# Optimization experiments

Measured on AMD Instinct MI355X. Metric: run time of the kernel, lower is better.

The kernel has to match this reference:

```python
import jax, jax.numpy as jnp
import numpy as np

N_HEADS = 16

def _rotate_half(t):
    # t: [B, H, T, hs]; split last dim in half, return cat(-x2, x1)
    hs = t.shape[-1]
    x1, x2 = t[..., : hs // 2], t[..., hs // 2 :]
    return jnp.concatenate((-x2, x1), axis=-1)

def _rope_pos(T, hs, dtype):
    inv_freq = 1.0 / (10000.0 ** (jnp.arange(0, hs, 2, dtype=jnp.float32) / hs))
    freqs = jnp.arange(T, dtype=jnp.float32)[:, None] * inv_freq[None, :]  # [T, hs/2]
    pos = jnp.concatenate((freqs, freqs), axis=-1)  # [T, hs]
    return pos

def setup_inputs() -> dict:
    key = jax.random.key(0)
    ks = jax.random.split(key, 5)
    d = 2048
    x = jax.random.normal(ks[0], (2, 2048, d), dtype=jnp.float32)
    W_attn = jax.random.normal(ks[1], (d, 3 * d), dtype=jnp.float32) * (1.0 / np.sqrt(d))
    b_attn = jax.random.normal(ks[2], (3 * d,), dtype=jnp.float32) * 0.02
    W_proj = jax.random.normal(ks[3], (d, d), dtype=jnp.float32) * (1.0 / np.sqrt(d))
    b_proj = jax.random.normal(ks[4], (d,), dtype=jnp.float32) * 0.02
    return {"x": x, "W_attn": W_attn, "b_attn": b_attn, "W_proj": W_proj, "b_proj": b_proj}

def reference(x, W_attn, b_attn, W_proj, b_proj):
    B, T, C = x.shape
    nh = N_HEADS
    hs = C // nh
    qkv = x @ W_attn + b_attn  # [B, T, 3C]
    q, k, v = jnp.split(qkv, 3, axis=-1)
    # [B, T, C] -> [B, nh, T, hs]
    def to_heads(t):
        return t.reshape(B, T, nh, hs).transpose(0, 2, 1, 3)
    q, k, v = to_heads(q), to_heads(k), to_heads(v)
    # RoPE
    pos = _rope_pos(T, hs, x.dtype)  # [T, hs]
    cos, sin = jnp.cos(pos).astype(x.dtype), jnp.sin(pos).astype(x.dtype)
    q = q * cos + _rotate_half(q) * sin
    k = k * cos + _rotate_half(k) * sin
    # causal SDPA
    scale = 1.0 / np.sqrt(hs)
    scores = jnp.einsum('bhqd,bhkd->bhqk', q, k) * scale  # [B, nh, T, T]
    causal = jnp.tril(jnp.ones((T, T), dtype=bool))
    scores = jnp.where(causal, scores, jnp.finfo(scores.dtype).min)
    att = jax.nn.softmax(scores, axis=-1)
    out = jnp.einsum('bhqk,bhkd->bhqd', att, v)  # [B, nh, T, hs]
    y = out.transpose(0, 2, 1, 3).reshape(B, T, C)
    return y @ W_proj + b_proj
```

## Files before the change

kernel.cpp:

```cpp
#include <hip/hip_runtime.h>
#include <stdint.h>

typedef unsigned short u16;
typedef __attribute__((ext_vector_type(8))) short short8;
typedef __attribute__((ext_vector_type(4))) float f32x4;
typedef __attribute__((ext_vector_type(4))) unsigned short u16x4;

#define DEV __device__ __forceinline__

DEV u16 f2bf(float f) {
  union { float f; unsigned u; } v; v.f = f;
  unsigned r = v.u + 0x7fffu + ((v.u >> 16) & 1u);
  return (u16)(r >> 16);
}
DEV float bf2f(u16 b) {
  union { unsigned u; float f; } v; v.u = ((unsigned)b) << 16;
  return v.f;
}
DEV void gload_lds16(const void* g, void* l) {
  __builtin_amdgcn_global_load_lds((const __attribute__((address_space(1))) void*)g,
                                   (__attribute__((address_space(3))) void*)l,
                                   16, 0, 0);
}
DEV void block_barrier() {
  asm volatile("" ::: "memory");
  __builtin_amdgcn_s_barrier();
  asm volatile("" ::: "memory");
}

__global__ void k_prep(const float* __restrict__ x, u16* __restrict__ xb,
                       const float* __restrict__ Wa, u16* __restrict__ wqkvT,
                       const float* __restrict__ Wp, u16* __restrict__ wprojT,
                       float* __restrict__ ct, float* __restrict__ st) {
  __shared__ float tile[32][33];
  const int bid = blockIdx.x, tid = threadIdx.x;
  if (bid < 8192) {
    int i = bid * 256 + tid;
    const f32x4 v = *(const f32x4*)(x + (size_t)i * 4);
    u16x4 o;
    o[0] = f2bf(v[0]); o[1] = f2bf(v[1]); o[2] = f2bf(v[2]); o[3] = f2bf(v[3]);
    *(u16x4*)(xb + (size_t)i * 4) = o;
  } else if (bid < 8192 + 12288 + 4096) {
    const bool wa = bid < 8192 + 12288;
    const int b2 = wa ? bid - 8192 : bid - 8192 - 12288;
    const int gw = wa ? 192 : 64;
    const float* in = wa ? Wa : Wp;
    u16* out = wa ? wqkvT : wprojT;
    const int C = wa ? 6144 : 2048;
    const int c0 = (b2 % gw) * 32, r0 = (b2 / gw) * 32;
    const int tx = tid & 31, ty = tid >> 5;
#pragma unroll
    for (int j = 0; j < 32; j += 8)
      tile[ty + j][tx] = in[(size_t)(r0 + ty + j) * C + (c0 + tx)];
    __syncthreads();
#pragma unroll
    for (int j = 0; j < 32; j += 8)
      out[(size_t)(c0 + ty + j) * 2048 + (r0 + tx)] = f2bf(tile[tx][ty + j]);
  } else {
    int id = (bid - 24576) * 256 + tid;
    int t = id >> 6, dd = id & 63;
    float inv = exp2f((float)dd * -0.20762050593045077f);
    float s, c;
    sincosf((float)t * inv, &s, &c);
    ct[id] = c; st[id] = s;
  }
}

__global__ __launch_bounds__(512, 2) void k_gemmqkv(const u16* __restrict__ A,
                                                    const u16* __restrict__ Bt,
                                                    const float* __restrict__ bias,
                                                    u16* __restrict__ qh,
                                                    u16* __restrict__ kh,
                                                    u16* __restrict__ vt,
                                                    const float* __restrict__ rtab) {
  const int Kld = 2048, nt = 32;
  __shared__ __align__(16) short smem[4][256 * 64];
  const int tid = threadIdx.x;
  const int wid = tid >> 6, lane = tid & 63;
  const int gx = gridDim.x;
  const int nwg = gx * gridDim.y;
  const int orig = blockIdx.y * gx + blockIdx.x;
  const int lg = (orig & 7) * (nwg >> 3) + (orig >> 3);
  const int bm = (lg % gx) * 256, bn = (lg / gx) * 256;
  const int wr = wid >> 2, wc = wid & 3;
  const int r = lane & 15, kq = lane >> 4, r7 = lane & 7;

  int aoff[4], boff[4], lbase[4];
#pragma unroll
  for (int j = 0; j < 4; ++j) {
    int c = j * 512 + wid * 64 + lane;
    int row = c >> 3, ch = c & 7;
    aoff[j] = (bm + row) * Kld + (ch ^ (row & 7)) * 8;
    boff[j] = (bn + row) * Kld + (ch ^ (row & 7)) * 8;
    lbase[j] = (j * 512 + wid * 64) * 16;
  }

#define STG_A(k0, buf, j) gload_lds16(A + aoff[j] + (k0), (char*)&smem[(buf)][0] + lbase[j])
#define STG_B(k0, buf, j) gload_lds16(Bt + boff[j] + (k0), (char*)&smem[2 + (buf)][0] + lbase[j])
#define RD_A(AF, MH, KK)                                                        \
  _Pragma("unroll")                                                             \
  for (int m2 = 0; m2 < 4; ++m2)                                                \
    AF[m2] = *(const short8*)&As[(wr * 128 + (MH) * 64 + m2 * 16 + r) * 64      \
                                 + (((KK) * 4 + kq) ^ r7) * 8];
#define RD_B(KK)                                                                \
  _Pragma("unroll")                                                             \
  for (int nf = 0; nf < 4; ++nf)                                                \
    bfr[KK][nf] = *(const short8*)&Bs[(wc * 64 + nf * 16 + r) * 64              \
                                      + (((KK) * 4 + kq) ^ r7) * 8];
#define PH_MFMA(AF, MH, KK)                                                     \
  __builtin_amdgcn_s_setprio(1);                                                \
  _Pragma("unroll")                                                             \
  for (int m2 = 0; m2 < 4; ++m2)                                                \
    _Pragma("unroll")                                                           \
    for (int nf = 0; nf < 4; ++nf)                                              \
      acc[(MH) * 4 + m2][nf] = __builtin_amdgcn_mfma_f32_16x16x32_bf16(         \
          AF[m2], bfr[KK][nf], acc[(MH) * 4 + m2][nf], 0, 0, 0);                \
  __builtin_amdgcn_s_setprio(0);

  f32x4 acc[8][4];
  const f32x4 zero = {0.f, 0.f, 0.f, 0.f};
#pragma unroll
  for (int i = 0; i < 8; ++i)
#pragma unroll
    for (int j = 0; j < 4; ++j) acc[i][j] = zero;

#pragma unroll
  for (int j = 0; j < 4; ++j) STG_A(0, 0, j);
#pragma unroll
  for (int j = 0; j < 4; ++j) STG_B(0, 0, j);
#pragma unroll
  for (int j = 0; j < 4; ++j) STG_B(64, 1, j);
  asm volatile("s_waitcnt vmcnt(4)" ::: "memory");
  block_barrier();

#pragma unroll 1
  for (int t = 0; t < nt; ++t) {
    const int cur = t & 1, nxt = cur ^ 1;
    const short* As = &smem[cur][0];
    const short* Bs = &smem[2 + cur][0];
    const int kA = (t + 1) * 64, kB = (t + 2) * 64;
    const bool sA = (t + 1 < nt), sB = (t + 2 < nt);
    short8 bfr[2][4];
    short8 af[4];

    RD_B(0)
    RD_A(af, 0, 0)
    if (sA) { STG_A(kA, nxt, 0); STG_A(kA, nxt, 1); }
    block_barrier();
    PH_MFMA(af, 0, 0)
    block_barrier();

    RD_B(1)
    RD_A(af, 0, 1)
    if (sA) { STG_A(kA, nxt, 2); STG_A(kA, nxt, 3); }
    block_barrier();
    PH_MFMA(af, 0, 1)
    block_barrier();

    RD_A(af, 1, 0)
    if (sB) { STG_B(kB, cur, 0); STG_B(kB, cur, 1); }
    block_barrier();
    PH_MFMA(af, 1, 0)
    block_barrier();

    RD_A(af, 1, 1)
    if (sB) { STG_B(kB, cur, 2); STG_B(kB, cur, 3); }
    block_barrier();
    PH_MFMA(af, 1, 1)
    if (t + 1 < nt) {
      if (sB) asm volatile("s_waitcnt vmcnt(4)" ::: "memory");
      else    asm volatile("s_waitcnt vmcnt(0)" ::: "memory");
    }
    block_barrier();
  }
#undef STG_A
#undef STG_B
#undef RD_A
#undef RD_B
#undef PH_MFMA

  const int by = lg / gx;
  const int part = by >> 3;
  const int b_ = bm >> 11;
  const int tb = bm & 2047;
  const int hbase = (bn & 2047) >> 7;
  u16* ob = (u16*)&smem[0][0];

#pragma unroll
  for (int nf = 0; nf < 4; ++nf) {
    int nl = wc * 64 + nf * 16 + r;
    float bv = bias[bn + nl];
#pragma unroll
    for (int mf = 0; mf < 8; ++mf) {
      int mlb = wr * 128 + mf * 16 + kq * 4;
#pragma unroll
      for (int i = 0; i < 4; ++i) {
        int ml = mlb + i;
        int cl = (part == 2)
          ? (nl ^ (((ml >> 2) & 3) << 4) ^ (((ml >> 4) & 7) << 1))
          : (nl ^ (((ml >> 2) & 3) << 4));
        ob[ml * 256 + cl] = f2bf(acc[mf][nf][i] + bv);
      }
    }
  }
  block_barrier();

  if (part == 2) {
#pragma unroll 1
    for (int iter = 0; iter < 32; ++iter) {
      int dl = iter * 8 + wid;
      int hh = hbase + (dl >> 7), d = dl & 127;
      int tl4 = lane * 4;
      int cl = dl ^ ((lane & 3) << 4) ^ (((lane >> 2) & 7) << 1);
      u16x4 o;
#pragma unroll
      for (int j = 0; j < 4; ++j) o[j] = ob[(tl4 + j) * 256 + cl];
      *(u16x4*)(vt + ((size_t)(b_ * 16 + hh) * 128 + d) * 2048 + tb + tl4) = o;
    }
  } else {
    u16* dst = part ? kh : qh;
    const float qscale = part ? 1.0f : 0.12751744766834352f;
    const int nl2 = lane * 4;
    const int hh = hbase + (nl2 >> 7);
    const int d0 = nl2 & 127;
    const int hi = (nl2 >> 6) & 1;
    const int dd4 = nl2 & 63;
    const float* ct = rtab;
    const float* st = rtab + 131072;
#pragma unroll 2
    for (int iter = 0; iter < 32; ++iter) {
      int tl = iter * 8 + wid;
      int tg = tb + tl;
      f32x4 c4 = *(const f32x4*)(ct + tg * 64 + dd4);
      f32x4 s4 = *(const f32x4*)(st + tg * 64 + dd4);
      int xr = ((tl >> 2) & 3) << 4;
      int base = tl * 256 + (nl2 ^ xr);
      int pbase = tl * 256 + ((nl2 ^ 64) ^ xr);
      u16x4 o;
#pragma unroll
      for (int j = 0; j < 4; ++j) {
        float vo = bf2f(ob[base + j]);
        float vp = bf2f(ob[pbase + j]);
        float vr = hi ? (vo * c4[j] + vp * s4[j]) : (vo * c4[j] - vp * s4[j]);
        o[j] = f2bf(vr * qscale);
      }
      *(u16x4*)(dst + ((size_t)(b_ * 16 + hh) * 2048 + tg) * 128 + d0) = o;
    }
  }
}

template <bool OUT_BF16, bool SPLITK>
__global__ __launch_bounds__(512, 2) void k_gemm3(const u16* __restrict__ A,
                                                  const u16* __restrict__ Bt,
                                                  const float* __restrict__ bias,
                                                  void* __restrict__ Cv,
                                                  int M, int N, int Kld, int nkt) {
  __shared__ __align__(16) short lA[2][256 * 64];
  __shared__ __align__(16) short lB[2][256 * 64];
  const int tid = threadIdx.x;
  const int wid = tid >> 6, lane = tid & 63;
  const int gx = gridDim.x;
  const int nwg = gx * gridDim.y;
  const int orig = blockIdx.y * gx + blockIdx.x;
  const int lg = (orig & 7) * (nwg >> 3) + (orig >> 3);
  const int bm = (lg % gx) * 256, bn = (lg / gx) * 256;
  const int wr = wid >> 2, wc = wid & 3;
  const int r = lane & 15, kq = lane >> 4, r7 = lane & 7;
  const int kz = SPLITK ? blockIdx.z * (nkt << 6) : 0;

  int aoff[4], boff[4], lbase[4];
#pragma unroll
  for (int j = 0; j < 4; ++j) {
    int c = j * 512 + wid * 64 + lane;
    int row = c >> 3, ch = c & 7;
    aoff[j] = (bm + row) * Kld + kz + (ch ^ (row & 7)) * 8;
    boff[j] = (bn + row) * Kld + kz + (ch ^ (row & 7)) * 8;
    lbase[j] = (j * 512 + wid * 64) * 16;
  }

#define STG_A(k0, buf, j) gload_lds16(A + aoff[j] + (k0), (char*)&lA[(buf)][0] + lbase[j])
#define STG_B(k0, buf, j) gload_lds16(Bt + boff[j] + (k0), (char*)&lB[(buf)][0] + lbase[j])
#define RD_A(AF, MH, KK)                                                        \
  _Pragma("unroll")                                                             \
  for (int m2 = 0; m2 < 4; ++m2)                                                \
    AF[m2] = *(const short8*)&As[(wr * 128 + (MH) * 64 + m2 * 16 + r) * 64      \
                                 + (((KK) * 4 + kq) ^ r7) * 8];
#define RD_B(KK)                                                                \
  _Pragma("unroll")                                                             \
  for (int nf = 0; nf < 4; ++nf)                                                \
    bfr[KK][nf] = *(const short8*)&Bs[(wc * 64 + nf * 16 + r) * 64              \
                                      + (((KK) * 4 + kq) ^ r7) * 8];
#define PH_MFMA(AF, MH, KK)                                                     \
  __builtin_amdgcn_s_setprio(1);                                                \
  _Pragma("unroll")                                                             \
  for (int m2 = 0; m2 < 4; ++m2)                                                \
    _Pragma("unroll")                                                           \
    for (int nf = 0; nf < 4; ++nf)                                              \
      acc[(MH) * 4 + m2][nf] = __builtin_amdgcn_mfma_f32_16x16x32_bf16(         \
          AF[m2], bfr[KK][nf], acc[(MH) * 4 + m2][nf], 0, 0, 0);                \
  __builtin_amdgcn_s_setprio(0);

  f32x4 acc[8][4];
  const f32x4 zero = {0.f, 0.f, 0.f, 0.f};
#pragma unroll
  for (int i = 0; i < 8; ++i)
#pragma unroll
    for (int j = 0; j < 4; ++j) acc[i][j] = zero;

  const int nt = nkt;

#pragma unroll
  for (int j = 0; j < 4; ++j) STG_A(0, 0, j);
#pragma unroll
  for (int j = 0; j < 4; ++j) STG_B(0, 0, j);
  if (nt > 1) {
#pragma unroll
    for (int j = 0; j < 4; ++j) STG_B(64, 1, j);
    asm volatile("s_waitcnt vmcnt(4)" ::: "memory");
  } else {
    asm volatile("s_waitcnt vmcnt(0)" ::: "memory");
  }
  block_barrier();

#pragma unroll 1
  for (int t = 0; t < nt; ++t) {
    const int cur = t & 1, nxt = cur ^ 1;
    const short* As = &lA[cur][0];
    const short* Bs = &lB[cur][0];
    const int kA = (t + 1) * 64, kB = (t + 2) * 64;
    const bool sA = (t + 1 < nt), sB = (t + 2 < nt);
    short8 bfr[2][4];
    short8 af[4];

    RD_B(0)
    RD_A(af, 0, 0)
    if (sA) { STG_A(kA, nxt, 0); STG_A(kA, nxt, 1); }
    block_barrier();
    PH_MFMA(af, 0, 0)
    block_barrier();

    RD_B(1)
    RD_A(af, 0, 1)
    if (sA) { STG_A(kA, nxt, 2); STG_A(kA, nxt, 3); }
    block_barrier();
    PH_MFMA(af, 0, 1)
    block_barrier();

    RD_A(af, 1, 0)
    if (sB) { STG_B(kB, cur, 0); STG_B(kB, cur, 1); }
    block_barrier();
    PH_MFMA(af, 1, 0)
    block_barrier();

    RD_A(af, 1, 1)
    if (sB) { STG_B(kB, cur, 2); STG_B(kB, cur, 3); }
    block_barrier();
    PH_MFMA(af, 1, 1)
    if (t + 1 < nt) {
      if (sB) asm volatile("s_waitcnt vmcnt(4)" ::: "memory");
      else    asm volatile("s_waitcnt vmcnt(0)" ::: "memory");
    }
    block_barrier();
  }
#undef STG_A
#undef STG_B
#undef RD_A
#undef RD_B
#undef PH_MFMA

#pragma unroll
  for (int mf = 0; mf < 8; ++mf)
#pragma unroll
    for (int nf = 0; nf < 4; ++nf) {
      int n = bn + wc * 64 + nf * 16 + r;
      float bv = SPLITK ? 0.f : bias[n];
#pragma unroll
      for (int i = 0; i < 4; ++i) {
        int m = bm + wr * 128 + mf * 16 + kq * 4 + i;
        float val = acc[mf][nf][i] + bv;
        if (SPLITK)
          ((float*)Cv)[(size_t)blockIdx.z * M * N + (size_t)m * N + n] = val;
        else if (OUT_BF16)
          ((u16*)Cv)[(size_t)m * N + n] = f2bf(val);
        else
          ((float*)Cv)[(size_t)m * N + n] = val;
      }
    }
}

__global__ void k_fadd(const float* __restrict__ p, const float* __restrict__ bias,
                       float* __restrict__ y, int n4) {
  const int half4 = 2097152;
  for (int i = blockIdx.x * blockDim.x + threadIdx.x; i < n4; i += gridDim.x * blockDim.x) {
    f32x4 a = *(const f32x4*)(p + (size_t)i * 4);
    f32x4 b = *(const f32x4*)(p + (size_t)(i + half4) * 4);
    f32x4 bv = *(const f32x4*)(bias + ((i & 511) << 2));
    f32x4 o = a + b + bv;
    *(f32x4*)(y + (size_t)i * 4) = o;
  }
}

__global__ __launch_bounds__(256) void k_attn(const u16* __restrict__ qh,
                                              const u16* __restrict__ kh,
                                              const u16* __restrict__ vt,
                                              u16* __restrict__ out) {
  __shared__ __align__(16) short lK[2][64 * 128];
  __shared__ __align__(16) short lV[2][128 * 64];
  __shared__ __align__(16) short lP[128 * 64];
  const int tid = threadIdx.x, wid = tid >> 6, lane = tid & 63;
  const int id = blockIdx.x;
  const int jr = id & 15;
  const int J = (id < 256) ? jr : 15 - jr;
  const int h = (id >> 4) & 15, b = id >> 8;
  const int q0 = J * 128;
  const int nkt = 2 * J + 2;
  const size_t bh = (size_t)b * 16 + h;
  const u16* qb = qh + bh * 2048 * 128;
  const u16* kb = kh + bh * 2048 * 128;
  const u16* vb = vt + bh * 128 * 2048;
  const int r = lane & 15, kq = lane >> 4;
  const int r7 = r & 7;
  const int wrow = wid * 32;

  int koff[4], voff[4];
#pragma unroll
  for (int i = 0; i < 4; ++i) {
    int ci = (wid * 4 + i) * 64 + lane;
    int krow = ci >> 4, kch = ci & 15;
    koff[i] = krow * 128 + ((kch ^ (krow & 7)) * 8);
    int vrow = ci >> 3, vch = ci & 7;
    voff[i] = vrow * 2048 + ((vch ^ (vrow & 7)) * 8);
  }

  short8 qa[2][4];
#pragma unroll
  for (int mf = 0; mf < 2; ++mf)
#pragma unroll
    for (int kk = 0; kk < 4; ++kk)
      qa[mf][kk] = *(const short8*)(qb + (size_t)(q0 + wrow + mf * 16 + r) * 128 + kk * 32 + kq * 8);

  f32x4 O[2][8];
  const f32x4 zero = {0.f, 0.f, 0.f, 0.f};
#pragma unroll
  for (int mf = 0; mf < 2; ++mf)
#pragma unroll
    for (int nf = 0; nf < 8; ++nf) O[mf][nf] = zero;
  float lp[2] = {0.f, 0.f};

#pragma unroll
  for (int i = 0; i < 4; ++i) {
    gload_lds16(kb + koff[i], (char*)&lK[0][0] + (wid * 4 + i) * 1024);
    gload_lds16(vb + voff[i], (char*)&lV[0][0] + (wid * 4 + i) * 1024);
  }

#pragma unroll 1
  for (int kt = 0; kt < nkt; ++kt) {
    const int cur = kt & 1;
    if (kt + 1 < nkt) {
      const size_t kbase = (size_t)(kt + 1) * 8192, vbase = (size_t)(kt + 1) * 64;
#pragma unroll
      for (int i = 0; i < 4; ++i) {
        gload_lds16(kb + kbase + koff[i], (char*)&lK[cur ^ 1][0] + (wid * 4 + i) * 1024);
        gload_lds16(vb + vbase + voff[i], (char*)&lV[cur ^ 1][0] + (wid * 4 + i) * 1024);
      }
      asm volatile("s_waitcnt vmcnt(8)" ::: "memory");
    } else {
      asm volatile("s_waitcnt vmcnt(0)" ::: "memory");
    }
    block_barrier();

    f32x4 S[2][4];
#pragma unroll
    for (int mf = 0; mf < 2; ++mf)
#pragma unroll
      for (int nf = 0; nf < 4; ++nf) S[mf][nf] = zero;
#pragma unroll
    for (int kk = 0; kk < 4; ++kk) {
      short8 kf[4];
#pragma unroll
      for (int nf = 0; nf < 4; ++nf)
        kf[nf] = *(const short8*)&lK[cur][(nf * 16 + r) * 128 + ((kk * 4 + kq) ^ r7) * 8];
      __builtin_amdgcn_s_setprio(1);
#pragma unroll
      for (int mf = 0; mf < 2; ++mf)
#pragma unroll
        for (int nf = 0; nf < 4; ++nf)
          S[mf][nf] = __builtin_amdgcn_mfma_f32_16x16x32_bf16(kf[nf], qa[mf][kk], S[mf][nf], 0, 0, 0);
      __builtin_amdgcn_s_setprio(0);
    }

    const bool diag = (kt >= nkt - 2);
#pragma unroll
    for (int mf = 0; mf < 2; ++mf) {
      const int rl = wrow + mf * 16 + r;
#pragma unroll
      for (int nf = 0; nf < 4; ++nf) {
        float pv4[4];
#pragma unroll
        for (int i = 0; i < 4; ++i) {
          float pv = exp2f(S[mf][nf][i]);
          if (diag) {
            int kg = kt * 64 + nf * 16 + kq * 4 + i;
            int qg = q0 + wrow + mf * 16 + r;
            pv = (kg > qg) ? 0.f : pv;
          }
          lp[mf] += pv;
          pv4[i] = pv;
        }
        unsigned d0, d1;
        asm("v_cvt_pk_bf16_f32 %0, %1, %2" : "=v"(d0) : "v"(pv4[0]), "v"(pv4[1]));
        asm("v_cvt_pk_bf16_f32 %0, %1, %2" : "=v"(d1) : "v"(pv4[2]), "v"(pv4[3]));
        int g = (nf * 4 + kq) ^ (r7 << 1);
        *(uint2*)((char*)lP + rl * 128 + g * 8) = make_uint2(d0, d1);
      }
    }

#pragma unroll
    for (int kk = 0; kk < 2; ++kk) {
      short8 pa[2];
#pragma unroll
      for (int mf = 0; mf < 2; ++mf) {
        int rl = wrow + mf * 16 + r;
        int g = (kk * 8 + kq * 2) ^ (r7 << 1);
        pa[mf] = *(const short8*)((const char*)lP + rl * 128 + g * 8);
      }
#pragma unroll
      for (int nf = 0; nf < 8; ++nf) {
        short8 vf = *(const short8*)&lV[cur][(nf * 16 + r) * 64 + ((kk * 4 + kq) ^ r7) * 8];
        __builtin_amdgcn_s_setprio(1);
#pragma unroll
        for (int mf = 0; mf < 2; ++mf)
          O[mf][nf] = __builtin_amdgcn_mfma_f32_16x16x32_bf16(pa[mf], vf, O[mf][nf], 0, 0, 0);
        __builtin_amdgcn_s_setprio(0);
      }
    }
    asm volatile("s_waitcnt lgkmcnt(0)" ::: "memory");
    block_barrier();
  }

#pragma unroll
  for (int mf = 0; mf < 2; ++mf) {
    float v = lp[mf];
    v += __shfl_xor(v, 16);
    v += __shfl_xor(v, 32);
    lp[mf] = v;
  }
#pragma unroll
  for (int mf = 0; mf < 2; ++mf) {
    float inv[4];
#pragma unroll
    for (int i = 0; i < 4; ++i)
      inv[i] = 1.f / __shfl(lp[mf], kq * 4 + i, 16);
#pragma unroll
    for (int nf = 0; nf < 8; ++nf)
#pragma unroll
      for (int i = 0; i < 4; ++i) {
        int qg = q0 + wrow + mf * 16 + kq * 4 + i;
        out[(size_t)(b * 2048 + qg) * 2048 + h * 128 + nf * 16 + r] = f2bf(O[mf][nf][i] * inv[i]);
      }
  }
}

extern "C" void kernel_launch(void* const* d_in, const int* in_sizes, int n_in,
                              void* d_out, int out_size, void* d_ws, size_t ws_size,
                              hipStream_t stream) {
  const float* x      = (const float*)d_in[0];
  const float* W_attn = (const float*)d_in[1];
  const float* b_attn = (const float*)d_in[2];
  const float* W_proj = (const float*)d_in[3];
  const float* b_proj = (const float*)d_in[4];
  float* y = (float*)d_out;

  u16* xb     = (u16*)d_ws;
  u16* wqkvT  = xb     + (size_t)4096 * 2048;
  u16* wprojT = wqkvT  + (size_t)6144 * 2048;
  u16* qkv    = wprojT + (size_t)2048 * 2048;
  u16* qh     = qkv    + (size_t)4096 * 6144;
  u16* kh     = qh     + (size_t)4096 * 2048;
  u16* vt     = kh     + (size_t)4096 * 2048;
  u16* attout = vt     + (size_t)4096 * 2048;
  if (ws_size < (size_t)83886080 * 2) return;

  float* rtab  = (float*)qkv;
  float* pproj = (float*)qkv;

  k_prep<<<25088, 256, 0, stream>>>(x, xb, W_attn, wqkvT, W_proj, wprojT, rtab, rtab + 131072);
  k_gemmqkv<<<dim3(16, 24), 512, 0, stream>>>(xb, wqkvT, b_attn, qh, kh, vt, rtab);
  k_attn<<<512, 256, 0, stream>>>(qh, kh, vt, attout);
  k_gemm3<false, true><<<dim3(16, 8, 2), 512, 0, stream>>>(attout, wprojT, b_proj, pproj, 4096, 2048, 2048, 16);
  k_fadd<<<2048, 256, 0, stream>>>(pproj, b_proj, y, 2097152);
}
```

Measured before the change: 300.6 us.

## Replace split-K projection GEMM plus reduction with 256x128-tile direct-output kernel

The output projection used to run as a split-K GEMM with 256x256 tiles that wrote two fp32 partial buffers, followed by a separate kernel that summed them and added the bias. It is now a single GEMM over the full K with 256x128 tiles on a 16x16 grid, adding the bias and writing y directly. This removes the partial-sum round trip through memory and one kernel launch. In exchange each tile reuses less data per load and runs a longer K loop.

Result: faster. 291.5 us (-3.0%).

```diff
diff --git a/kernel.cpp b/kernel.cpp
--- a/kernel.cpp
+++ b/kernel.cpp
@@ -249,41 +249,43 @@
   }
 }
 
-template <bool OUT_BF16, bool SPLITK>
-__global__ __launch_bounds__(512, 2) void k_gemm3(const u16* __restrict__ A,
-                                                  const u16* __restrict__ Bt,
-                                                  const float* __restrict__ bias,
-                                                  void* __restrict__ Cv,
-                                                  int M, int N, int Kld, int nkt) {
+__global__ __launch_bounds__(512, 2) void k_proj(const u16* __restrict__ A,
+                                                 const u16* __restrict__ Bt,
+                                                 const float* __restrict__ bias,
+                                                 float* __restrict__ y) {
+  const int Kld = 2048, nt = 32;
   __shared__ __align__(16) short lA[2][256 * 64];
-  __shared__ __align__(16) short lB[2][256 * 64];
+  __shared__ __align__(16) short lB[2][128 * 64];
   const int tid = threadIdx.x;
   const int wid = tid >> 6, lane = tid & 63;
-  const int gx = gridDim.x;
-  const int nwg = gx * gridDim.y;
-  const int orig = blockIdx.y * gx + blockIdx.x;
-  const int lg = (orig & 7) * (nwg >> 3) + (orig >> 3);
-  const int bm = (lg % gx) * 256, bn = (lg / gx) * 256;
-  const int wr = wid >> 2, wc = wid & 3;
+  const int orig = blockIdx.y * 16 + blockIdx.x;
+  const int lg = (orig & 7) * 32 + (orig >> 3);
+  const int bm = (lg & 15) * 256, bn = (lg >> 4) * 128;
+  const int wr = wid >> 1, wc = wid & 1;
   const int r = lane & 15, kq = lane >> 4, r7 = lane & 7;
-  const int kz = SPLITK ? blockIdx.z * (nkt << 6) : 0;
-
-  int aoff[4], boff[4], lbase[4];
+
+  int aoff[4], boff[2], albase[4], blbase[2];
 #pragma unroll
   for (int j = 0; j < 4; ++j) {
     int c = j * 512 + wid * 64 + lane;
     int row = c >> 3, ch = c & 7;
-    aoff[j] = (bm + row) * Kld + kz + (ch ^ (row & 7)) * 8;
-    boff[j] = (bn + row) * Kld + kz + (ch ^ (row & 7)) * 8;
-    lbase[j] = (j * 512 + wid * 64) * 16;
-  }
-
-#define STG_A(k0, buf, j) gload_lds16(A + aoff[j] + (k0), (char*)&lA[(buf)][0] + lbase[j])
-#define STG_B(k0, buf, j) gload_lds16(Bt + boff[j] + (k0), (char*)&lB[(buf)][0] + lbase[j])
+    aoff[j] = (bm + row) * Kld + (ch ^ (row & 7)) * 8;
+    albase[j] = (j * 512 + wid * 64) * 16;
+  }
+#pragma unroll
+  for (int j = 0; j < 2; ++j) {
+    int c = j * 512 + wid * 64 + lane;
+    int row = c >> 3, ch = c & 7;
+    boff[j] = (bn + row) * Kld + (ch ^ (row & 7)) * 8;
+    blbase[j] = (j * 512 + wid * 64) * 16;
+  }
+
+#define STG_A(k0, buf, j) gload_lds16(A + aoff[j] + (k0), (char*)&lA[(buf)][0] + albase[j])
+#define STG_B(k0, buf, j) gload_lds16(Bt + boff[j] + (k0), (char*)&lB[(buf)][0] + blbase[j])
 #define RD_A(AF, MH, KK)                                                        \
   _Pragma("unroll")                                                             \
-  for (int m2 = 0; m2 < 4; ++m2)                                                \
-    AF[m2] = *(const short8*)&As[(wr * 128 + (MH) * 64 + m2 * 16 + r) * 64      \
+  for (int m2 = 0; m2 < 2; ++m2)                                                \
+    AF[m2] = *(const short8*)&As[(wr * 64 + (MH) * 32 + m2 * 16 + r) * 64       \
                                  + (((KK) * 4 + kq) ^ r7) * 8];
 #define RD_B(KK)                                                                \
   _Pragma("unroll")                                                             \
@@ -293,33 +295,27 @@
 #define PH_MFMA(AF, MH, KK)                                                     \
   __builtin_amdgcn_s_setprio(1);                                                \
   _Pragma("unroll")                                                             \
-  for (int m2 = 0; m2 < 4; ++m2)                                                \
+  for (int m2 = 0; m2 < 2; ++m2)                                                \
     _Pragma("unroll")                                                           \
     for (int nf = 0; nf < 4; ++nf)                                              \
-      acc[(MH) * 4 + m2][nf] = __builtin_amdgcn_mfma_f32_16x16x32_bf16(         \
-          AF[m2], bfr[KK][nf], acc[(MH) * 4 + m2][nf], 0, 0, 0);                \
+      acc[(MH) * 2 + m2][nf] = __builtin_amdgcn_mfma_f32_16x16x32_bf16(         \
+          AF[m2], bfr[KK][nf], acc[(MH) * 2 + m2][nf], 0, 0, 0);                \
   __builtin_amdgcn_s_setprio(0);
 
-  f32x4 acc[8][4];
+  f32x4 acc[4][4];
   const f32x4 zero = {0.f, 0.f, 0.f, 0.f};
 #pragma unroll
-  for (int i = 0; i < 8; ++i)
+  for (int i = 0; i < 4; ++i)
 #pragma unroll
     for (int j = 0; j < 4; ++j) acc[i][j] = zero;
 
-  const int nt = nkt;
-
 #pragma unroll
   for (int j = 0; j < 4; ++j) STG_A(0, 0, j);
 #pragma unroll
-  for (int j = 0; j < 4; ++j) STG_B(0, 0, j);
-  if (nt > 1) {
-#pragma unroll
-    for (int j = 0; j < 4; ++j) STG_B(64, 1, j);
-    asm volatile("s_waitcnt vmcnt(4)" ::: "memory");
-  } else {
-    asm volatile("s_waitcnt vmcnt(0)" ::: "memory");
-  }
+  for (int j = 0; j < 2; ++j) STG_B(0, 0, j);
+#pragma unroll
+  for (int j = 0; j < 2; ++j) STG_B(64, 1, j);
+  asm volatile("s_waitcnt vmcnt(2)" ::: "memory");
   block_barrier();
 
 #pragma unroll 1
@@ -330,7 +326,7 @@
     const int kA = (t + 1) * 64, kB = (t + 2) * 64;
     const bool sA = (t + 1 < nt), sB = (t + 2 < nt);
     short8 bfr[2][4];
-    short8 af[4];
+    short8 af[2];
 
     RD_B(0)
     RD_A(af, 0, 0)
@@ -347,17 +343,17 @@
     block_barrier();
 
     RD_A(af, 1, 0)
-    if (sB) { STG_B(kB, cur, 0); STG_B(kB, cur, 1); }
+    if (sB) STG_B(kB, cur, 0);
     block_barrier();
     PH_MFMA(af, 1, 0)
     block_barrier();
 
     RD_A(af, 1, 1)
-    if (sB) { STG_B(kB, cur, 2); STG_B(kB, cur, 3); }
+    if (sB) STG_B(kB, cur, 1);
     block_barrier();
     PH_MFMA(af, 1, 1)
     if (t + 1 < nt) {
-      if (sB) asm volatile("s_waitcnt vmcnt(4)" ::: "memory");
+      if (sB) asm volatile("s_waitcnt vmcnt(2)" ::: "memory");
       else    asm volatile("s_waitcnt vmcnt(0)" ::: "memory");
     }
     block_barrier();
@@ -369,35 +365,17 @@
 #undef PH_MFMA
 
 #pragma unroll
-  for (int mf = 0; mf < 8; ++mf)
+  for (int mf = 0; mf < 4; ++mf)
 #pragma unroll
     for (int nf = 0; nf < 4; ++nf) {
       int n = bn + wc * 64 + nf * 16 + r;
-      float bv = SPLITK ? 0.f : bias[n];
+      float bv = bias[n];
 #pragma unroll
       for (int i = 0; i < 4; ++i) {
-        int m = bm + wr * 128 + mf * 16 + kq * 4 + i;
-        float val = acc[mf][nf][i] + bv;
-        if (SPLITK)
-          ((float*)Cv)[(size_t)blockIdx.z * M * N + (size_t)m * N + n] = val;
-        else if (OUT_BF16)
-          ((u16*)Cv)[(size_t)m * N + n] = f2bf(val);
-        else
-          ((float*)Cv)[(size_t)m * N + n] = val;
-      }
-    }
-}
-
-__global__ void k_fadd(const float* __restrict__ p, const float* __restrict__ bias,
-                       float* __restrict__ y, int n4) {
-  const int half4 = 2097152;
-  for (int i = blockIdx.x * blockDim.x + threadIdx.x; i < n4; i += gridDim.x * blockDim.x) {
-    f32x4 a = *(const f32x4*)(p + (size_t)i * 4);
-    f32x4 b = *(const f32x4*)(p + (size_t)(i + half4) * 4);
-    f32x4 bv = *(const f32x4*)(bias + ((i & 511) << 2));
-    f32x4 o = a + b + bv;
-    *(f32x4*)(y + (size_t)i * 4) = o;
-  }
+        int m = bm + wr * 64 + mf * 16 + kq * 4 + i;
+        y[(size_t)m * 2048 + n] = acc[mf][nf][i] + bv;
+      }
+    }
 }
 
 __global__ __launch_bounds__(256) void k_attn(const u16* __restrict__ qh,
@@ -581,12 +559,10 @@
   u16* attout = vt     + (size_t)4096 * 2048;
   if (ws_size < (size_t)83886080 * 2) return;
 
-  float* rtab  = (float*)qkv;
-  float* pproj = (float*)qkv;
+  float* rtab = (float*)qkv;
 
   k_prep<<<25088, 256, 0, stream>>>(x, xb, W_attn, wqkvT, W_proj, wprojT, rtab, rtab + 131072);
   k_gemmqkv<<<dim3(16, 24), 512, 0, stream>>>(xb, wqkvT, b_attn, qh, kh, vt, rtab);
   k_attn<<<512, 256, 0, stream>>>(qh, kh, vt, attout);
-  k_gemm3<false, true><<<dim3(16, 8, 2), 512, 0, stream>>>(attout, wprojT, b_proj, pproj, 4096, 2048, 2048, 16);
-  k_fadd<<<2048, 256, 0, stream>>>(pproj, b_proj, y, 2097152);
-}
+  k_proj<<<dim3(16, 16), 512, 0, stream>>>(attout, wprojT, b_proj, y);
+}
```
